# Kernel tuning notes

Measured on AMD Instinct MI355X. Metric: run time of the kernel, lower is better.

The kernel has to match this reference:

```python
import jax, jax.numpy as jnp
import numpy as np

LINHAS, COLUNAS, DIM, BATCH = 32, 32, 256, 2048
NEURONS = LINHAS * COLUNAS
TAXA_INICIAL = 0.5
SIGMA_INICIAL = max(LINHAS, COLUNAS) / 2.0  # 16.0


def _grid_locs():
    # matches tf.meshgrid default 'xy' indexing, stacked then flattened
    x = jnp.arange(LINHAS, dtype=jnp.float32)
    y = jnp.arange(COLUNAS, dtype=jnp.float32)
    g = jnp.stack(jnp.meshgrid(x, y), axis=-1)  # (COLUNAS, LINHAS, 2)
    return g.reshape(-1, 2)


def setup_inputs() -> dict:
    key = jax.random.key(0)
    k1, k2 = jax.random.split(key)
    X = jax.random.normal(k1, (BATCH, DIM), dtype=jnp.float32)
    # keras 'random_normal' initializer: stddev 0.05
    pesos = jax.random.normal(k2, (NEURONS, DIM), dtype=jnp.float32) * 0.05
    return {
        "X": X,
        "pesos": pesos,
        "localizacoes": _grid_locs(),
        "passo_atual": 100,
        "total_passos": 1000,
    }


def reference(X, pesos, localizacoes, passo_atual, total_passos):
    frac = jnp.float32(passo_atual) / jnp.float32(total_passos)
    taxa = TAXA_INICIAL * jnp.exp(-frac)
    sigma = SIGMA_INICIAL * jnp.exp(-frac)

    # squared-euclidean distances (B, N)
    x2 = jnp.sum(X * X, axis=1, keepdims=True)
    w2 = jnp.sum(pesos * pesos, axis=1)
    dist = x2 + w2 - 2.0 * (X @ pesos.T)

    bmu_idx = jnp.argmin(dist, axis=1)            # (B,)
    bmu_loc = localizacoes[bmu_idx]               # (B, 2)

    # grid distances and Gaussian neighborhood (B, N)
    dist_grade = jnp.sum((localizacoes[None, :, :] - bmu_loc[:, None, :]) ** 2, axis=2)
    h = jnp.exp(-dist_grade / (2.0 * sigma ** 2))

    # delta_total = mean_b taxa * h[b,n] * (X[b,d] - W[n,d]), computed without
    # materializing the (B, N, D) tensor:
    B = jnp.float32(X.shape[0])
    delta_total = taxa * (jnp.einsum('bn,bd->nd', h, X) - jnp.sum(h, axis=0)[:, None] * pesos) / B

    new_pesos = pesos + delta_total
    return new_pesos
```

## Files before the change

### kernel.cpp

```cpp
#include <hip/hip_runtime.h>
#include <float.h>

#define Bsz 2048
#define Nn  1024
#define Dd  256

typedef __attribute__((ext_vector_type(8))) short bf16x8;
typedef __attribute__((ext_vector_type(4))) float f32x4;
typedef unsigned long long u64;

__device__ __forceinline__ unsigned short bfr(float x) {
    unsigned u = __float_as_uint(x);
    u += 0x7fffu + ((u >> 16) & 1u);
    return (unsigned short)(u >> 16);
}
__device__ __forceinline__ float bf2f(unsigned short h) {
    return __uint_as_float(((unsigned)h) << 16);
}

__device__ __forceinline__ void som_params(const int* __restrict__ step,
                                           const int* __restrict__ total,
                                           float* taxa, float* inv2s2) {
    float frac = (float)(*step) / (float)(*total);
    float e = __expf(-frac);
    *taxa = 0.5f * e;
    float sigma = 16.0f * e;
    *inv2s2 = 1.0f / (2.0f * sigma * sigma);
}

__device__ __forceinline__ u64 packsc(float f, int n) {
    unsigned u = __float_as_uint(f);
    u = (u & 0x80000000u) ? ~u : (u | 0x80000000u);
    return ((u64)u << 32) | (unsigned)n;
}

__global__ __launch_bounds__(256) void prep_w(
    const float* __restrict__ W, ushort* __restrict__ hi,
    ushort* __restrict__ lo, float* __restrict__ w2)
{
    int row  = blockIdx.x * 4 + (threadIdx.x >> 6);
    int lane = threadIdx.x & 63;
    float4 v = ((const float4*)(W + (size_t)row * Dd))[lane];
    float s = v.x*v.x + v.y*v.y + v.z*v.z + v.w*v.w;
    #pragma unroll
    for (int m = 32; m; m >>= 1) s += __shfl_xor(s, m, 64);
    if (lane == 0) w2[row] = s;
    ushort4 h, l;
    h.x = bfr(v.x); l.x = bfr(v.x - bf2f(h.x));
    h.y = bfr(v.y); l.y = bfr(v.y - bf2f(h.y));
    h.z = bfr(v.z); l.z = bfr(v.z - bf2f(h.z));
    h.w = bfr(v.w); l.w = bfr(v.w - bf2f(h.w));
    *(ushort4*)&hi[(size_t)row * Dd + lane * 4] = h;
    *(ushort4*)&lo[(size_t)row * Dd + lane * 4] = l;
}

__global__ __launch_bounds__(256) void prep_x(
    const float* __restrict__ X, ushort* __restrict__ Xhi,
    ushort* __restrict__ Xlo, ushort* __restrict__ Xt,
    u64* __restrict__ bmin)
{
    __shared__ float ld[64][65];
    const int t  = threadIdx.x;
    const int b0 = blockIdx.x * 64;
    const int d0 = blockIdx.y * 64;

    if (blockIdx.y == 0 && t < 64) bmin[b0 + t] = ~0ull;

    #pragma unroll
    for (int p = 0; p < 4; ++p) {
        int flat = p * 256 + t;
        int row = flat >> 4, c4 = flat & 15;
        float4 v = *(const float4*)&X[(size_t)(b0 + row) * Dd + d0 + c4 * 4];
        ushort4 h, l;
        h.x = bfr(v.x); l.x = bfr(v.x - bf2f(h.x));
        h.y = bfr(v.y); l.y = bfr(v.y - bf2f(h.y));
        h.z = bfr(v.z); l.z = bfr(v.z - bf2f(h.z));
        h.w = bfr(v.w); l.w = bfr(v.w - bf2f(h.w));
        size_t off = (size_t)(b0 + row) * Dd + d0 + c4 * 4;
        *(ushort4*)&Xhi[off] = h;
        *(ushort4*)&Xlo[off] = l;
        ld[row][c4*4+0] = v.x; ld[row][c4*4+1] = v.y;
        ld[row][c4*4+2] = v.z; ld[row][c4*4+3] = v.w;
    }
    __syncthreads();
    #pragma unroll
    for (int q = 0; q < 2; ++q) {
        int idx = q * 256 + t;
        int d = idx >> 3;
        int bs = (idx & 7) * 8;
        bf16x8 o;
        #pragma unroll
        for (int j = 0; j < 8; ++j) o[j] = (short)bfr(ld[bs + j][d]);
        *(bf16x8*)&Xt[(size_t)(d0 + d) * Bsz + b0 + bs] = o;
    }
}

__global__ __launch_bounds__(256) void bmu_mfma(
    const ushort* __restrict__ Xhi, const ushort* __restrict__ Xlo,
    const ushort* __restrict__ Whi, const ushort* __restrict__ Wlo,
    const float* __restrict__ w2, u64* __restrict__ bmin)
{
    const int t = threadIdx.x, w = t >> 6, l = t & 63;
    const int wm = w & 1, wn = w >> 1;
    const int b0 = blockIdx.x * 128 + wm * 64;
    const int n0 = blockIdx.y * 64 + wn * 32;
    const int lr = l & 15, lg = l >> 4;

    f32x4 acc[4][2];
    #pragma unroll
    for (int m = 0; m < 4; ++m)
        #pragma unroll
        for (int n = 0; n < 2; ++n) { f32x4 z = {0.f,0.f,0.f,0.f}; acc[m][n] = z; }

    #pragma unroll
    for (int kd = 0; kd < Dd; kd += 32) {
        bf16x8 ah[4], al[4], bh[2], bl[2];
        #pragma unroll
        for (int m = 0; m < 4; ++m) {
            size_t off = (size_t)(b0 + m*16 + lr) * Dd + kd + lg*8;
            ah[m] = *(const bf16x8*)&Xhi[off];
            al[m] = *(const bf16x8*)&Xlo[off];
        }
        #pragma unroll
        for (int n = 0; n < 2; ++n) {
            size_t off = (size_t)(n0 + n*16 + lr) * Dd + kd + lg*8;
            bh[n] = *(const bf16x8*)&Whi[off];
            bl[n] = *(const bf16x8*)&Wlo[off];
        }
        #pragma unroll
        for (int m = 0; m < 4; ++m)
            #pragma unroll
            for (int n = 0; n < 2; ++n) {
                acc[m][n] = __builtin_amdgcn_mfma_f32_16x16x32_bf16(ah[m], bh[n], acc[m][n], 0, 0, 0);
                acc[m][n] = __builtin_amdgcn_mfma_f32_16x16x32_bf16(ah[m], bl[n], acc[m][n], 0, 0, 0);
                acc[m][n] = __builtin_amdgcn_mfma_f32_16x16x32_bf16(al[m], bh[n], acc[m][n], 0, 0, 0);
            }
    }

    float w2v[2]; int nidx[2];
    #pragma unroll
    for (int n = 0; n < 2; ++n) { nidx[n] = n0 + n*16 + lr; w2v[n] = w2[nidx[n]]; }

    #pragma unroll
    for (int m = 0; m < 4; ++m)
        #pragma unroll
        for (int r = 0; r < 4; ++r) {
            u64 p0 = packsc(w2v[0] - 2.f * acc[m][0][r], nidx[0]);
            u64 p1 = packsc(w2v[1] - 2.f * acc[m][1][r], nidx[1]);
            u64 pm = p1 < p0 ? p1 : p0;
            #pragma unroll
            for (int msk = 1; msk < 16; msk <<= 1) {
                unsigned lo = (unsigned)pm, hi = (unsigned)(pm >> 32);
                lo = __shfl_xor(lo, msk, 64);
                hi = __shfl_xor(hi, msk, 64);
                u64 o = ((u64)hi << 32) | lo;
                if (o < pm) pm = o;
            }
            if (lr == 0) {
                int b = b0 + m*16 + lg*4 + r;
                atomicMin(&bmin[b], pm);
            }
        }
}

__global__ __launch_bounds__(256) void hgen(
    const u64* __restrict__ bmin, const int* __restrict__ step,
    const int* __restrict__ total, ushort* __restrict__ Ht,
    float* __restrict__ hsum)
{
    const int n = blockIdx.x, t = threadIdx.x;
    float taxa, inv2s2;
    som_params(step, total, &taxa, &inv2s2);
    const int nx = n & 31, ny = n >> 5;

    float part = 0.f;
    bf16x8 o;
    #pragma unroll
    for (int j = 0; j < 8; ++j) {
        unsigned idx = (unsigned)(bmin[t*8 + j] & 0xffffffffu);
        int dx = nx - (int)(idx & 31);
        int dy = ny - (int)(idx >> 5);
        float h = __expf(-(float)(dx*dx + dy*dy) * inv2s2);
        o[j] = (short)bfr(h);
        part += h;
    }
    *(bf16x8*)&Ht[(size_t)n * Bsz + t*8] = o;

    #pragma unroll
    for (int m = 1; m < 64; m <<= 1) part += __shfl_xor(part, m, 64);
    __shared__ float ws[4];
    if ((t & 63) == 0) ws[t >> 6] = part;
    __syncthreads();
    if (t == 0) hsum[n] = ws[0] + ws[1] + ws[2] + ws[3];
}

__global__ __launch_bounds__(512) void acc_finish(
    const ushort* __restrict__ Ht, const ushort* __restrict__ Xt,
    const float* __restrict__ hsum, const float* __restrict__ W,
    const int* __restrict__ step, const int* __restrict__ total,
    float* __restrict__ out)
{
    __shared__ float red[8][32][36];

    const int t = threadIdx.x, w = t >> 6, l = t & 63;
    const int lr = l & 15, lg = l >> 4;
    const int n0 = blockIdx.x * 32;
    const int d0 = blockIdx.y * 32;

    f32x4 acc[2][2];
    #pragma unroll
    for (int m = 0; m < 2; ++m)
        #pragma unroll
        for (int nf = 0; nf < 2; ++nf) { f32x4 z = {0.f,0.f,0.f,0.f}; acc[m][nf] = z; }

    #pragma unroll
    for (int ks = 0; ks < 8; ++ks) {
        const int bk = w * 256 + ks * 32 + lg * 8;
        bf16x8 am[2], bx[2];
        #pragma unroll
        for (int m = 0; m < 2; ++m)
            am[m] = *(const bf16x8*)&Ht[(size_t)(n0 + m*16 + lr) * Bsz + bk];
        #pragma unroll
        for (int nf = 0; nf < 2; ++nf)
            bx[nf] = *(const bf16x8*)&Xt[(size_t)(d0 + nf*16 + lr) * Bsz + bk];
        #pragma unroll
        for (int m = 0; m < 2; ++m)
            #pragma unroll
            for (int nf = 0; nf < 2; ++nf)
                acc[m][nf] = __builtin_amdgcn_mfma_f32_16x16x32_bf16(am[m], bx[nf], acc[m][nf], 0, 0, 0);
    }

    #pragma unroll
    for (int m = 0; m < 2; ++m)
        #pragma unroll
        for (int nf = 0; nf < 2; ++nf)
            #pragma unroll
            for (int r = 0; r < 4; ++r)
                red[w][m*16 + lg*4 + r][nf*16 + lr] = acc[m][nf][r];
    __syncthreads();

    float taxa, inv2s2;
    som_params(step, total, &taxa, &inv2s2);
    const float invB = 1.0f / 2048.0f;

    const int nl = t >> 4;
    const int dl = (t & 15) * 2;
    float s0 = 0.f, s1 = 0.f;
    #pragma unroll
    for (int ww = 0; ww < 8; ++ww) {
        s0 += red[ww][nl][dl];
        s1 += red[ww][nl][dl + 1];
    }
    const int n = n0 + nl;
    const int d = d0 + dl;
    const float hsn = hsum[n];
    const float* wp = &W[(size_t)n * Dd + d];
    float wv0 = wp[0], wv1 = wp[1];
    float o0 = wv0 + taxa * (s0 - hsn * wv0) * invB;
    float o1 = wv1 + taxa * (s1 - hsn * wv1) * invB;
    float2 o = make_float2(o0, o1);
    *(float2*)&out[(size_t)n * Dd + d] = o;
}

extern "C" void kernel_launch(void* const* d_in, const int* in_sizes, int n_in,
                              void* d_out, int out_size, void* d_ws, size_t ws_size,
                              hipStream_t stream)
{
    const float* X    = (const float*)d_in[0];
    const float* W    = (const float*)d_in[1];
    const int* step   = (const int*)d_in[3];
    const int* total  = (const int*)d_in[4];
    float* out = (float*)d_out;

    char* p = (char*)d_ws;
    float* w2   = (float*)p;  p += 4096;
    u64*   bmin = (u64*)p;    p += 16384;
    float* hsum = (float*)p;  p += 4096;
    ushort* Xt  = (ushort*)p; p += 1048576;
    char* regA = p;
    ushort* Xhi = (ushort*)regA;
    ushort* Xlo = (ushort*)(regA + 1048576);
    ushort* Whi = (ushort*)(regA + 2097152);
    ushort* Wlo = (ushort*)(regA + 2621440);
    ushort* Ht  = (ushort*)regA;

    prep_w    <<<256, 256, 0, stream>>>(W, Whi, Wlo, w2);
    prep_x    <<<dim3(32, 4), 256, 0, stream>>>(X, Xhi, Xlo, Xt, bmin);
    bmu_mfma  <<<dim3(16, 16), 256, 0, stream>>>(Xhi, Xlo, Whi, Wlo, w2, bmin);
    hgen      <<<1024, 256, 0, stream>>>(bmin, step, total, Ht, hsum);
    acc_finish<<<dim3(32, 8), 512, 0, stream>>>(Ht, Xt, hsum, W, step, total, out);
}
```

Measured before the change: 44.32 us.

## Merge prep kernels and compute neighborhood weights inside accumulation kernel

New measurement: 37.22 us. 16.0% less time.

```diff
diff --git a/kernel.cpp b/kernel.cpp
--- a/kernel.cpp
+++ b/kernel.cpp
@@ -34,64 +34,66 @@
     return ((u64)u << 32) | (unsigned)n;
 }
 
-__global__ __launch_bounds__(256) void prep_w(
-    const float* __restrict__ W, ushort* __restrict__ hi,
-    ushort* __restrict__ lo, float* __restrict__ w2)
-{
-    int row  = blockIdx.x * 4 + (threadIdx.x >> 6);
-    int lane = threadIdx.x & 63;
-    float4 v = ((const float4*)(W + (size_t)row * Dd))[lane];
-    float s = v.x*v.x + v.y*v.y + v.z*v.z + v.w*v.w;
-    #pragma unroll
-    for (int m = 32; m; m >>= 1) s += __shfl_xor(s, m, 64);
-    if (lane == 0) w2[row] = s;
-    ushort4 h, l;
-    h.x = bfr(v.x); l.x = bfr(v.x - bf2f(h.x));
-    h.y = bfr(v.y); l.y = bfr(v.y - bf2f(h.y));
-    h.z = bfr(v.z); l.z = bfr(v.z - bf2f(h.z));
-    h.w = bfr(v.w); l.w = bfr(v.w - bf2f(h.w));
-    *(ushort4*)&hi[(size_t)row * Dd + lane * 4] = h;
-    *(ushort4*)&lo[(size_t)row * Dd + lane * 4] = l;
-}
-
-__global__ __launch_bounds__(256) void prep_x(
-    const float* __restrict__ X, ushort* __restrict__ Xhi,
-    ushort* __restrict__ Xlo, ushort* __restrict__ Xt,
+__global__ __launch_bounds__(256) void prep_all(
+    const float* __restrict__ X, const float* __restrict__ W,
+    ushort* __restrict__ Xhi, ushort* __restrict__ Xlo,
+    ushort* __restrict__ Whi, ushort* __restrict__ Wlo,
+    ushort* __restrict__ Xt, float* __restrict__ w2,
     u64* __restrict__ bmin)
 {
     __shared__ float ld[64][65];
-    const int t  = threadIdx.x;
-    const int b0 = blockIdx.x * 64;
-    const int d0 = blockIdx.y * 64;
-
-    if (blockIdx.y == 0 && t < 64) bmin[b0 + t] = ~0ull;
-
-    #pragma unroll
-    for (int p = 0; p < 4; ++p) {
-        int flat = p * 256 + t;
-        int row = flat >> 4, c4 = flat & 15;
-        float4 v = *(const float4*)&X[(size_t)(b0 + row) * Dd + d0 + c4 * 4];
-        ushort4 h, l;
-        h.x = bfr(v.x); l.x = bfr(v.x - bf2f(h.x));
-        h.y = bfr(v.y); l.y = bfr(v.y - bf2f(h.y));
-        h.z = bfr(v.z); l.z = bfr(v.z - bf2f(h.z));
-        h.w = bfr(v.w); l.w = bfr(v.w - bf2f(h.w));
-        size_t off = (size_t)(b0 + row) * Dd + d0 + c4 * 4;
-        *(ushort4*)&Xhi[off] = h;
-        *(ushort4*)&Xlo[off] = l;
-        ld[row][c4*4+0] = v.x; ld[row][c4*4+1] = v.y;
-        ld[row][c4*4+2] = v.z; ld[row][c4*4+3] = v.w;
-    }
-    __syncthreads();
-    #pragma unroll
-    for (int q = 0; q < 2; ++q) {
-        int idx = q * 256 + t;
-        int d = idx >> 3;
-        int bs = (idx & 7) * 8;
-        bf16x8 o;
-        #pragma unroll
-        for (int j = 0; j < 8; ++j) o[j] = (short)bfr(ld[bs + j][d]);
-        *(bf16x8*)&Xt[(size_t)(d0 + d) * Bsz + b0 + bs] = o;
+    const int t = threadIdx.x;
+    const int bid = blockIdx.x;
+
+    if (bid < 256) {
+        int row  = bid * 4 + (t >> 6);
+        int lane = t & 63;
+        float4 v = ((const float4*)(W + (size_t)row * Dd))[lane];
+        float s = v.x*v.x + v.y*v.y + v.z*v.z + v.w*v.w;
+        #pragma unroll
+        for (int m = 32; m; m >>= 1) s += __shfl_xor(s, m, 64);
+        if (lane == 0) w2[row] = s;
+        ushort4 h4, l4;
+        h4.x = bfr(v.x); l4.x = bfr(v.x - bf2f(h4.x));
+        h4.y = bfr(v.y); l4.y = bfr(v.y - bf2f(h4.y));
+        h4.z = bfr(v.z); l4.z = bfr(v.z - bf2f(h4.z));
+        h4.w = bfr(v.w); l4.w = bfr(v.w - bf2f(h4.w));
+        *(ushort4*)&Whi[(size_t)row * Dd + lane * 4] = h4;
+        *(ushort4*)&Wlo[(size_t)row * Dd + lane * 4] = l4;
+    } else {
+        const int idx = bid - 256;
+        const int b0 = (idx & 31) * 64;
+        const int d0 = (idx >> 5) * 64;
+
+        if ((idx >> 5) == 0 && t < 64) bmin[b0 + t] = ~0ull;
+
+        #pragma unroll
+        for (int p = 0; p < 4; ++p) {
+            int flat = p * 256 + t;
+            int row = flat >> 4, c4 = flat & 15;
+            float4 v = *(const float4*)&X[(size_t)(b0 + row) * Dd + d0 + c4 * 4];
+            ushort4 h4, l4;
+            h4.x = bfr(v.x); l4.x = bfr(v.x - bf2f(h4.x));
+            h4.y = bfr(v.y); l4.y = bfr(v.y - bf2f(h4.y));
+            h4.z = bfr(v.z); l4.z = bfr(v.z - bf2f(h4.z));
+            h4.w = bfr(v.w); l4.w = bfr(v.w - bf2f(h4.w));
+            size_t off = (size_t)(b0 + row) * Dd + d0 + c4 * 4;
+            *(ushort4*)&Xhi[off] = h4;
+            *(ushort4*)&Xlo[off] = l4;
+            ld[row][c4*4+0] = v.x; ld[row][c4*4+1] = v.y;
+            ld[row][c4*4+2] = v.z; ld[row][c4*4+3] = v.w;
+        }
+        __syncthreads();
+        #pragma unroll
+        for (int q = 0; q < 2; ++q) {
+            int idx2 = q * 256 + t;
+            int d  = idx2 >> 3;
+            int bs = (idx2 & 7) * 8;
+            bf16x8 o;
+            #pragma unroll
+            for (int j = 0; j < 8; ++j) o[j] = (short)bfr(ld[bs + j][d]);
+            *(bf16x8*)&Xt[(size_t)(d0 + d) * Bsz + b0 + bs] = o;
+        }
     }
 }
 
@@ -150,10 +152,10 @@
             u64 pm = p1 < p0 ? p1 : p0;
             #pragma unroll
             for (int msk = 1; msk < 16; msk <<= 1) {
-                unsigned lo = (unsigned)pm, hi = (unsigned)(pm >> 32);
-                lo = __shfl_xor(lo, msk, 64);
-                hi = __shfl_xor(hi, msk, 64);
-                u64 o = ((u64)hi << 32) | lo;
+                unsigned plo = (unsigned)pm, phi = (unsigned)(pm >> 32);
+                plo = __shfl_xor(plo, msk, 64);
+                phi = __shfl_xor(phi, msk, 64);
+                u64 o = ((u64)phi << 32) | plo;
                 if (o < pm) pm = o;
             }
             if (lr == 0) {
@@ -163,72 +165,61 @@
         }
 }
 
-__global__ __launch_bounds__(256) void hgen(
-    const u64* __restrict__ bmin, const int* __restrict__ step,
-    const int* __restrict__ total, ushort* __restrict__ Ht,
-    float* __restrict__ hsum)
-{
-    const int n = blockIdx.x, t = threadIdx.x;
-    float taxa, inv2s2;
-    som_params(step, total, &taxa, &inv2s2);
-    const int nx = n & 31, ny = n >> 5;
-
-    float part = 0.f;
-    bf16x8 o;
-    #pragma unroll
-    for (int j = 0; j < 8; ++j) {
-        unsigned idx = (unsigned)(bmin[t*8 + j] & 0xffffffffu);
-        int dx = nx - (int)(idx & 31);
-        int dy = ny - (int)(idx >> 5);
-        float h = __expf(-(float)(dx*dx + dy*dy) * inv2s2);
-        o[j] = (short)bfr(h);
-        part += h;
-    }
-    *(bf16x8*)&Ht[(size_t)n * Bsz + t*8] = o;
-
-    #pragma unroll
-    for (int m = 1; m < 64; m <<= 1) part += __shfl_xor(part, m, 64);
-    __shared__ float ws[4];
-    if ((t & 63) == 0) ws[t >> 6] = part;
-    __syncthreads();
-    if (t == 0) hsum[n] = ws[0] + ws[1] + ws[2] + ws[3];
-}
-
 __global__ __launch_bounds__(512) void acc_finish(
-    const ushort* __restrict__ Ht, const ushort* __restrict__ Xt,
-    const float* __restrict__ hsum, const float* __restrict__ W,
-    const int* __restrict__ step, const int* __restrict__ total,
-    float* __restrict__ out)
+    const ushort* __restrict__ Xt, const u64* __restrict__ bmin,
+    const float* __restrict__ W, const int* __restrict__ step,
+    const int* __restrict__ total, float* __restrict__ out)
 {
     __shared__ float red[8][32][36];
+    __shared__ float hws[8][32];
 
     const int t = threadIdx.x, w = t >> 6, l = t & 63;
     const int lr = l & 15, lg = l >> 4;
     const int n0 = blockIdx.x * 32;
     const int d0 = blockIdx.y * 32;
 
+    float taxa, inv2s2;
+    som_params(step, total, &taxa, &inv2s2);
+
+    const float fny  = (float)(n0 >> 5);
+    const float fnx0 = (float)lr;
+    const float fnx1 = (float)(lr + 16);
+
     f32x4 acc[2][2];
     #pragma unroll
     for (int m = 0; m < 2; ++m)
         #pragma unroll
         for (int nf = 0; nf < 2; ++nf) { f32x4 z = {0.f,0.f,0.f,0.f}; acc[m][nf] = z; }
+    float hs0 = 0.f, hs1 = 0.f;
 
     #pragma unroll
     for (int ks = 0; ks < 8; ++ks) {
         const int bk = w * 256 + ks * 32 + lg * 8;
-        bf16x8 am[2], bx[2];
-        #pragma unroll
-        for (int m = 0; m < 2; ++m)
-            am[m] = *(const bf16x8*)&Ht[(size_t)(n0 + m*16 + lr) * Bsz + bk];
-        #pragma unroll
-        for (int nf = 0; nf < 2; ++nf)
-            bx[nf] = *(const bf16x8*)&Xt[(size_t)(d0 + nf*16 + lr) * Bsz + bk];
-        #pragma unroll
-        for (int m = 0; m < 2; ++m)
-            #pragma unroll
-            for (int nf = 0; nf < 2; ++nf)
-                acc[m][nf] = __builtin_amdgcn_mfma_f32_16x16x32_bf16(am[m], bx[nf], acc[m][nf], 0, 0, 0);
-    }
+        bf16x8 am0, am1;
+        #pragma unroll
+        for (int j = 0; j < 8; ++j) {
+            unsigned idx = (unsigned)(bmin[bk + j] & 0xffffffffu);
+            float bx = (float)(idx & 31), by = (float)(idx >> 5);
+            float dy  = fny - by;
+            float dy2 = dy * dy;
+            float dx0 = fnx0 - bx, dx1 = fnx1 - bx;
+            float h0 = __expf(-(dx0*dx0 + dy2) * inv2s2);
+            float h1 = __expf(-(dx1*dx1 + dy2) * inv2s2);
+            am0[j] = (short)bfr(h0);
+            am1[j] = (short)bfr(h1);
+            hs0 += h0; hs1 += h1;
+        }
+        bf16x8 bx0 = *(const bf16x8*)&Xt[(size_t)(d0 + lr)      * Bsz + bk];
+        bf16x8 bx1 = *(const bf16x8*)&Xt[(size_t)(d0 + 16 + lr) * Bsz + bk];
+        acc[0][0] = __builtin_amdgcn_mfma_f32_16x16x32_bf16(am0, bx0, acc[0][0], 0, 0, 0);
+        acc[0][1] = __builtin_amdgcn_mfma_f32_16x16x32_bf16(am0, bx1, acc[0][1], 0, 0, 0);
+        acc[1][0] = __builtin_amdgcn_mfma_f32_16x16x32_bf16(am1, bx0, acc[1][0], 0, 0, 0);
+        acc[1][1] = __builtin_amdgcn_mfma_f32_16x16x32_bf16(am1, bx1, acc[1][1], 0, 0, 0);
+    }
+
+    hs0 += __shfl_xor(hs0, 16, 64); hs0 += __shfl_xor(hs0, 32, 64);
+    hs1 += __shfl_xor(hs1, 16, 64); hs1 += __shfl_xor(hs1, 32, 64);
+    if (l < 16) { hws[w][l] = hs0; hws[w][16 + l] = hs1; }
 
     #pragma unroll
     for (int m = 0; m < 2; ++m)
@@ -239,26 +230,22 @@
                 red[w][m*16 + lg*4 + r][nf*16 + lr] = acc[m][nf][r];
     __syncthreads();
 
-    float taxa, inv2s2;
-    som_params(step, total, &taxa, &inv2s2);
     const float invB = 1.0f / 2048.0f;
-
     const int nl = t >> 4;
     const int dl = (t & 15) * 2;
-    float s0 = 0.f, s1 = 0.f;
+    float s0 = 0.f, s1 = 0.f, hsn = 0.f;
     #pragma unroll
     for (int ww = 0; ww < 8; ++ww) {
-        s0 += red[ww][nl][dl];
-        s1 += red[ww][nl][dl + 1];
+        s0  += red[ww][nl][dl];
+        s1  += red[ww][nl][dl + 1];
+        hsn += hws[ww][nl];
     }
     const int n = n0 + nl;
     const int d = d0 + dl;
-    const float hsn = hsum[n];
     const float* wp = &W[(size_t)n * Dd + d];
     float wv0 = wp[0], wv1 = wp[1];
-    float o0 = wv0 + taxa * (s0 - hsn * wv0) * invB;
-    float o1 = wv1 + taxa * (s1 - hsn * wv1) * invB;
-    float2 o = make_float2(o0, o1);
+    float2 o = make_float2(wv0 + taxa * (s0 - hsn * wv0) * invB,
+                           wv1 + taxa * (s1 - hsn * wv1) * invB);
     *(float2*)&out[(size_t)n * Dd + d] = o;
 }
 
@@ -275,18 +262,13 @@
     char* p = (char*)d_ws;
     float* w2   = (float*)p;  p += 4096;
     u64*   bmin = (u64*)p;    p += 16384;
-    float* hsum = (float*)p;  p += 4096;
     ushort* Xt  = (ushort*)p; p += 1048576;
-    char* regA = p;
-    ushort* Xhi = (ushort*)regA;
-    ushort* Xlo = (ushort*)(regA + 1048576);
-    ushort* Whi = (ushort*)(regA + 2097152);
-    ushort* Wlo = (ushort*)(regA + 2621440);
-    ushort* Ht  = (ushort*)regA;
-
-    prep_w    <<<256, 256, 0, stream>>>(W, Whi, Wlo, w2);
-    prep_x    <<<dim3(32, 4), 256, 0, stream>>>(X, Xhi, Xlo, Xt, bmin);
+    ushort* Xhi = (ushort*)p; p += 1048576;
+    ushort* Xlo = (ushort*)p; p += 1048576;
+    ushort* Whi = (ushort*)p; p += 524288;
+    ushort* Wlo = (ushort*)p; p += 524288;
+
+    prep_all  <<<384, 256, 0, stream>>>(X, W, Xhi, Xlo, Whi, Wlo, Xt, w2, bmin);
     bmu_mfma  <<<dim3(16, 16), 256, 0, stream>>>(Xhi, Xlo, Whi, Wlo, w2, bmin);
-    hgen      <<<1024, 256, 0, stream>>>(bmin, step, total, Ht, hsum);
-    acc_finish<<<dim3(32, 8), 512, 0, stream>>>(Ht, Xt, hsum, W, step, total, out);
-}
+    acc_finish<<<dim3(32, 8), 512, 0, stream>>>(Xt, bmin, W, step, total, out);
+}
```
